# Performance work log

Hardware: AMD Instinct MI355X
Metric: run time of the kernel (lower is better)

Reference implementation:

```python
import jax, jax.numpy as jnp
import numpy as np


def _wkv_scan(key, value, time_decay, time_first):
    # Numerically-stabilized RWKV WKV recurrence; key/value: [B,T,C]
    w = -jnp.exp(time_decay)  # [C]
    B, T, C = key.shape

    def step(carry, kv):
        num, den, mx = carry
        k, v = kv  # [B,C] each
        # output at this timestep
        mo = jnp.maximum(mx, k + time_first)
        e1 = jnp.exp(mx - mo)
        e2 = jnp.exp(k + time_first - mo)
        out = (e1 * num + e2 * v) / (e1 * den + e2)
        # state update
        ms = jnp.maximum(mx + w, k)
        e1s = jnp.exp(mx + w - ms)
        e2s = jnp.exp(k - ms)
        return (e1s * num + e2s * v, e1s * den + e2s, ms), out

    init = (jnp.zeros((B, C), key.dtype),
            jnp.zeros((B, C), key.dtype),
            jnp.full((B, C), -1e38, key.dtype))
    kT = jnp.swapaxes(key, 0, 1)   # [T,B,C]
    vT = jnp.swapaxes(value, 0, 1)
    _, outs = jax.lax.scan(step, init, (kT, vT))
    return jnp.swapaxes(outs, 0, 1)  # [B,T,C]


def setup_inputs() -> dict:
    key = jax.random.key(0)
    ks = jax.random.split(key, 10)
    B, T, C = 8, 2048, 1024
    s = 1.0 / np.sqrt(C)
    return {
        "x": jax.random.normal(ks[0], (B, T, C), jnp.float32),
        "wk": jax.random.normal(ks[1], (C, C), jnp.float32) * s,
        "wv": jax.random.normal(ks[2], (C, C), jnp.float32) * s,
        "wr": jax.random.normal(ks[3], (C, C), jnp.float32) * s,
        "wo": jax.random.normal(ks[4], (C, C), jnp.float32) * s,
        "time_decay": jax.random.normal(ks[5], (C,), jnp.float32) * 0.5,
        "time_first": jax.random.normal(ks[6], (C,), jnp.float32) * 0.5,
        "mix_k": jax.random.uniform(ks[7], (1, 1, C), jnp.float32),
        "mix_v": jax.random.uniform(ks[8], (1, 1, C), jnp.float32),
        "mix_r": jax.random.uniform(ks[9], (1, 1, C), jnp.float32),
    }


def reference(x, wk, wv, wr, wo, time_decay, time_first, mix_k, mix_v, mix_r):
    # time_shift: prev_x[:,0]=0, prev_x[:,t]=x[:,t-1]  (ZeroPad2d((0,0,1,-1)))
    prev_x = jnp.pad(x, ((0, 0), (1, 0), (0, 0)))[:, :-1, :]
    k_in = x * mix_k + prev_x * (1.0 - mix_k)
    v_in = x * mix_v + prev_x * (1.0 - mix_v)
    r_in = x * mix_r + prev_x * (1.0 - mix_r)
    key = jnp.einsum('btc,dc->btd', k_in, wk)
    value = jnp.einsum('btc,dc->btd', v_in, wv)
    receptance = jax.nn.sigmoid(jnp.einsum('btc,dc->btd', r_in, wr))
    wkv = _wkv_scan(key, value, time_decay, time_first)
    rwkv = receptance * wkv
    return jnp.einsum('btc,dc->btd', rwkv, wo)
```

## Files before the change

### kernel.cpp

```cpp
#include <hip/hip_runtime.h>
#include <stdint.h>


using bf16x8 = __attribute__((ext_vector_type(8))) __bf16;
using f32x4  = __attribute__((ext_vector_type(4))) float;

union FU { float f; unsigned int u; };

__device__ __forceinline__ unsigned short f2b(float f) {
  FU v; v.f = f;
  unsigned int u = v.u;
  return (unsigned short)((u + 0x7fffu + ((u >> 16) & 1u)) >> 16);
}
__device__ __forceinline__ float b2f(unsigned short h) {
  FU v; v.u = ((unsigned int)h) << 16; return v.f;
}

__device__ __forceinline__ void gl_lds16(const unsigned short* g,
                                         const unsigned short* l) {
  __builtin_amdgcn_global_load_lds(
      (const __attribute__((address_space(1))) void*)g,
      (__attribute__((address_space(3))) void*)l, 16, 0, 0);
}

#define SBAR()  __builtin_amdgcn_s_barrier()
#define LGKM0() asm volatile("s_waitcnt lgkmcnt(0)")
#define VMW(n)  asm volatile("s_waitcnt vmcnt(" #n ")")

__global__ __launch_bounds__(256) void prep_kernel(
    const float* __restrict__ x,
    const float* __restrict__ w0, const float* __restrict__ w1,
    const float* __restrict__ w2, const float* __restrict__ w3,
    unsigned short* __restrict__ o0, unsigned short* __restrict__ o1,
    unsigned short* __restrict__ o2, unsigned short* __restrict__ o3,
    const float* __restrict__ mk, const float* __restrict__ mv,
    const float* __restrict__ mr,
    unsigned short* __restrict__ ok, unsigned short* __restrict__ ov,
    unsigned short* __restrict__ orr)
{
  int bid = blockIdx.x;
  if (bid < 4096) {
    int mat = bid >> 10, blk = bid & 1023;
    const float* src = (mat == 0) ? w0 : (mat == 1) ? w1 : (mat == 2) ? w2 : w3;
    unsigned short* dst = (mat == 0) ? o0 : (mat == 1) ? o1 : (mat == 2) ? o2 : o3;
    int i = blk * 1024 + threadIdx.x * 4;
    float4 v = *(const float4*)(src + i);
    union { int2 i2; unsigned short u[4]; } o;
    o.u[0] = f2b(v.x); o.u[1] = f2b(v.y); o.u[2] = f2b(v.z); o.u[3] = f2b(v.w);
    *(int2*)(dst + i) = o.i2;
    return;
  }
  int i = (bid - 4096) * 256 + threadIdx.x;
  int base = i * 8;
  int row = base >> 10;
  int t = row & 2047;
  int c = base & 1023;
  float xv[8], pv[8];
  *(float4*)&xv[0] = *(const float4*)(x + base);
  *(float4*)&xv[4] = *(const float4*)(x + base + 4);
  if (t > 0) {
    *(float4*)&pv[0] = *(const float4*)(x + base - 1024);
    *(float4*)&pv[4] = *(const float4*)(x + base - 1024 + 4);
  } else {
#pragma unroll
    for (int e = 0; e < 8; ++e) pv[e] = 0.f;
  }
  float mkv[8], mvv[8], mrv[8];
  *(float4*)&mkv[0] = *(const float4*)(mk + c);
  *(float4*)&mkv[4] = *(const float4*)(mk + c + 4);
  *(float4*)&mvv[0] = *(const float4*)(mv + c);
  *(float4*)&mvv[4] = *(const float4*)(mv + c + 4);
  *(float4*)&mrv[0] = *(const float4*)(mr + c);
  *(float4*)&mrv[4] = *(const float4*)(mr + c + 4);
  union { int4 i4; unsigned short u[8]; } a, b2, d;
#pragma unroll
  for (int e = 0; e < 8; ++e) {
    float xe = xv[e], pe = pv[e];
    a.u[e]  = f2b(xe * mkv[e] + pe * (1.f - mkv[e]));
    b2.u[e] = f2b(xe * mvv[e] + pe * (1.f - mvv[e]));
    d.u[e]  = f2b(xe * mrv[e] + pe * (1.f - mrv[e]));
  }
  *(int4*)(ok + base)  = a.i4;
  *(int4*)(ov + base)  = b2.i4;
  *(int4*)(orr + base) = d.i4;
}


__device__ __forceinline__ void stageHalf(
    const unsigned short* __restrict__ g,
    const unsigned short* l,
    int rh, int kt, int w, int rl, int koffel)
{
#pragma unroll
  for (int c = 0; c < 2; ++c) {
    int rows = rh * 128 + (2 * w + c) * 8;
    gl_lds16(g + (size_t)(rows + rl) * 1024 + kt * 64 + koffel,
             l + rows * 64);
  }
}

template<int Q>
__device__ __forceinline__ void quadMfma(f32x4 (&acc)[8][4],
    bf16x8 a00, bf16x8 a01, bf16x8 a10, bf16x8 a11, bf16x8 (&b)[4][2])
{
#pragma unroll
  for (int j = 0; j < 4; ++j) {
    acc[2*Q][j]   = __builtin_amdgcn_mfma_f32_16x16x32_bf16(a00, b[j][0], acc[2*Q][j],   0, 0, 0);
    acc[2*Q][j]   = __builtin_amdgcn_mfma_f32_16x16x32_bf16(a01, b[j][1], acc[2*Q][j],   0, 0, 0);
    acc[2*Q+1][j] = __builtin_amdgcn_mfma_f32_16x16x32_bf16(a10, b[j][0], acc[2*Q+1][j], 0, 0, 0);
    acc[2*Q+1][j] = __builtin_amdgcn_mfma_f32_16x16x32_bf16(a11, b[j][1], acc[2*Q+1][j], 0, 0, 0);
  }
}

template<bool ST_A, bool ST_B, int VMN>
__device__ __forceinline__ void ktile(
    const unsigned short* aR, const unsigned short* bR,
    const unsigned short* aW, const unsigned short* bW,
    const unsigned short* Am, const unsigned short* Wn,
    int ktA, int ktB, int w, int wm, int wn, int col, int quad,
    int swzel, int rl, int koffel, f32x4 (&acc)[8][4])
{
  const int ks0 = (quad * 8) ^ swzel;
  const int ks1 = (32 + quad * 8) ^ swzel;
  bf16x8 b[4][2];
#pragma unroll
  for (int j = 0; j < 4; ++j) {
    const unsigned short* br = bR + (wn * 64 + j * 16 + col) * 64;
    b[j][0] = *(const bf16x8*)(br + ks0);
    b[j][1] = *(const bf16x8*)(br + ks1);
  }
  const unsigned short* ar = aR + (wm * 128 + col) * 64;
  {
    bf16x8 a00 = *(const bf16x8*)(ar + 0 * 1024 + ks0);
    bf16x8 a01 = *(const bf16x8*)(ar + 0 * 1024 + ks1);
    bf16x8 a10 = *(const bf16x8*)(ar + 1 * 1024 + ks0);
    bf16x8 a11 = *(const bf16x8*)(ar + 1 * 1024 + ks1);
    if (ST_A) stageHalf(Am, aW, 0, ktA, w, rl, koffel);
    SBAR(); LGKM0();
    __builtin_amdgcn_s_setprio(1);
    quadMfma<0>(acc, a00, a01, a10, a11, b);
    __builtin_amdgcn_s_setprio(0);
    SBAR();
  }
  {
    bf16x8 a00 = *(const bf16x8*)(ar + 2 * 1024 + ks0);
    bf16x8 a01 = *(const bf16x8*)(ar + 2 * 1024 + ks1);
    bf16x8 a10 = *(const bf16x8*)(ar + 3 * 1024 + ks0);
    bf16x8 a11 = *(const bf16x8*)(ar + 3 * 1024 + ks1);
    if (ST_A) stageHalf(Am, aW, 1, ktA, w, rl, koffel);
    SBAR(); LGKM0();
    __builtin_amdgcn_s_setprio(1);
    quadMfma<1>(acc, a00, a01, a10, a11, b);
    __builtin_amdgcn_s_setprio(0);
    SBAR();
  }
  {
    bf16x8 a00 = *(const bf16x8*)(ar + 4 * 1024 + ks0);
    bf16x8 a01 = *(const bf16x8*)(ar + 4 * 1024 + ks1);
    bf16x8 a10 = *(const bf16x8*)(ar + 5 * 1024 + ks0);
    bf16x8 a11 = *(const bf16x8*)(ar + 5 * 1024 + ks1);
    if (ST_B) stageHalf(Wn, bW, 0, ktB, w, rl, koffel);
    SBAR(); LGKM0();
    __builtin_amdgcn_s_setprio(1);
    quadMfma<2>(acc, a00, a01, a10, a11, b);
    __builtin_amdgcn_s_setprio(0);
    SBAR();
  }
  {
    bf16x8 a00 = *(const bf16x8*)(ar + 6 * 1024 + ks0);
    bf16x8 a01 = *(const bf16x8*)(ar + 6 * 1024 + ks1);
    bf16x8 a10 = *(const bf16x8*)(ar + 7 * 1024 + ks0);
    bf16x8 a11 = *(const bf16x8*)(ar + 7 * 1024 + ks1);
    if (ST_B) stageHalf(Wn, bW, 1, ktB, w, rl, koffel);
    SBAR(); LGKM0();
    __builtin_amdgcn_s_setprio(1);
    quadMfma<3>(acc, a00, a01, a10, a11, b);
    __builtin_amdgcn_s_setprio(0);
    if constexpr (VMN == 4) { VMW(4); }
    else if constexpr (VMN == 0) { VMW(0); }
    SBAR();
  }
}

template<typename EPI>
__device__ __forceinline__ void gemm256(
    const unsigned short* __restrict__ A,
    const unsigned short* __restrict__ W,
    EPI epi)
{
  __shared__ __align__(16) unsigned short As[2][256 * 64];
  __shared__ __align__(16) unsigned short Bs[2][256 * 64];
  const int tid  = threadIdx.x;
  const int lane = tid & 63;
  const int w    = tid >> 6;
  const int wm   = w >> 2, wn = w & 3;
  const int col  = lane & 15, quad = lane >> 4;
  const int swzel  = (lane & 7) << 3;
  const int rl     = lane >> 3;
  const int koffel = ((lane & 7) ^ rl) << 3;
  const int mBase = blockIdx.x * 256;
  const int nBase = blockIdx.y * 256;
  const unsigned short* Am = A + (size_t)mBase * 1024;
  const unsigned short* Wn = W + (size_t)nBase * 1024;

  f32x4 acc[8][4];
  const f32x4 z = {0.f, 0.f, 0.f, 0.f};
#pragma unroll
  for (int i = 0; i < 8; ++i)
#pragma unroll
    for (int j = 0; j < 4; ++j) acc[i][j] = z;

  stageHalf(Wn, &Bs[0][0], 0, 0, w, rl, koffel);
  stageHalf(Wn, &Bs[0][0], 1, 0, w, rl, koffel);
  stageHalf(Am, &As[0][0], 0, 0, w, rl, koffel);
  stageHalf(Am, &As[0][0], 1, 0, w, rl, koffel);
  stageHalf(Wn, &Bs[1][0], 0, 1, w, rl, koffel);
  stageHalf(Wn, &Bs[1][0], 1, 1, w, rl, koffel);
  VMW(4); SBAR();

#pragma unroll 1
  for (int t = 0; t < 14; t += 2) {
    ktile<true, true, 4>(&As[0][0], &Bs[0][0], &As[1][0], &Bs[0][0],
                         Am, Wn, t + 1, t + 2,
                         w, wm, wn, col, quad, swzel, rl, koffel, acc);
    ktile<true, true, 4>(&As[1][0], &Bs[1][0], &As[0][0], &Bs[1][0],
                         Am, Wn, t + 2, t + 3,
                         w, wm, wn, col, quad, swzel, rl, koffel, acc);
  }
  ktile<true, false, 0>(&As[0][0], &Bs[0][0], &As[1][0], &Bs[0][0],
                        Am, Wn, 15, 0,
                        w, wm, wn, col, quad, swzel, rl, koffel, acc);
  ktile<false, false, -1>(&As[1][0], &Bs[1][0], &As[0][0], &Bs[1][0],
                          Am, Wn, 0, 0,
                          w, wm, wn, col, quad, swzel, rl, koffel, acc);

  const int mB = mBase + wm * 128, nB = nBase + wn * 64;
#pragma unroll
  for (int i = 0; i < 8; ++i)
#pragma unroll
    for (int j = 0; j < 4; ++j)
#pragma unroll
      for (int r = 0; r < 4; ++r)
        epi(mB + i * 16 + quad * 4 + r, nB + j * 16 + col, acc[i][j][r]);
}

__global__ __launch_bounds__(512, 2) void gemmKV2_kernel(
    const unsigned short* __restrict__ A0, const unsigned short* __restrict__ A1,
    const unsigned short* __restrict__ W0, const unsigned short* __restrict__ W1,
    unsigned short* __restrict__ out0, unsigned short* __restrict__ out1)
{
  const int z = blockIdx.z;
  const unsigned short* A = z ? A1 : A0;
  const unsigned short* W = z ? W1 : W0;
  unsigned short* out = z ? out1 : out0;
  gemm256(A, W, [&](int r, int c, float v) {
    out[(size_t)r * 1024 + c] = f2b(v);
  });
}

__global__ __launch_bounds__(512, 2) void gemmR2_kernel(
    const unsigned short* __restrict__ A, const unsigned short* __restrict__ W,
    unsigned short* __restrict__ out)
{
  gemm256(A, W, [&](int r, int c, float v) {
    out[(size_t)r * 1024 + c] = f2b(1.0f / (1.0f + __expf(-v)));
  });
}

__global__ __launch_bounds__(512, 2) void gemmO2_kernel(
    const unsigned short* __restrict__ A, const unsigned short* __restrict__ W,
    float* __restrict__ out)
{
  gemm256(A, W, [&](int r, int c, float v) {
    out[(size_t)r * 1024 + c] = v;
  });
}

__global__ __launch_bounds__(256) void wkv_pass1(
    const unsigned short* __restrict__ kb, const unsigned short* __restrict__ vb,
    const float* __restrict__ td,
    float* __restrict__ snum, float* __restrict__ sden, float* __restrict__ smx,
    int T, int C, int L)
{
  int g = blockIdx.x * 256 + threadIdx.x;
  int bc = g & 8191;
  int ch = g >> 13;
  int c = bc & 1023;
  float w = -__expf(td[c]);
  float num = 0.f, den = 0.f, mx = -1e38f;
  size_t base = ((size_t)(bc >> 10) * T + (size_t)ch * L) * C + c;
  for (int j0 = 0; j0 < L; j0 += 8) {
    float kq[8], vq[8];
#pragma unroll
    for (int j = 0; j < 8; ++j) {
      size_t a = base + (size_t)(j0 + j) * C;
      kq[j] = b2f(kb[a]);
      vq[j] = b2f(vb[a]);
    }
#pragma unroll
    for (int j = 0; j < 8; ++j) {
      float k = kq[j], v = vq[j];
      float mw = mx + w;
      float ms = fmaxf(mw, k);
      float s1 = __expf(mw - ms);
      float s2 = __expf(k - ms);
      num = s1 * num + s2 * v;
      den = s1 * den + s2;
      mx = ms;
    }
  }
  int idx = ch * 8192 + bc;
  snum[idx] = num; sden[idx] = den; smx[idx] = mx;
}

__global__ __launch_bounds__(64) void wkv_pass2(
    const float* __restrict__ snum, const float* __restrict__ sden,
    const float* __restrict__ smx, const float* __restrict__ td,
    float* __restrict__ inum, float* __restrict__ iden, float* __restrict__ imx,
    int L)
{
  int bc = blockIdx.x * 64 + threadIdx.x;
  int c = bc & 1023;
  float Wl = -__expf(td[c]) * (float)L;
  float num = 0.f, den = 0.f, mx = -1e38f;
#pragma unroll
  for (int ch = 0; ch < 32; ++ch) {
    int idx = ch * 8192 + bc;
    inum[idx] = num; iden[idx] = den; imx[idx] = mx;
    float sn = snum[idx], sd = sden[idx], sm = smx[idx];
    float mi = mx + Wl;
    float mo = fmaxf(mi, sm);
    float e1 = __expf(mi - mo);
    float e2 = __expf(sm - mo);
    num = e1 * num + e2 * sn;
    den = e1 * den + e2 * sd;
    mx = mo;
  }
}

__global__ __launch_bounds__(256) void wkv_pass3(
    const unsigned short* __restrict__ kb, const unsigned short* __restrict__ vb,
    const unsigned short* __restrict__ rsig,
    const float* __restrict__ td, const float* __restrict__ tf,
    const float* __restrict__ inum, const float* __restrict__ iden,
    const float* __restrict__ imx,
    unsigned short* __restrict__ rwkv, int T, int C, int L)
{
  int g = blockIdx.x * 256 + threadIdx.x;
  int bc = g & 8191;
  int ch = g >> 13;
  int c = bc & 1023;
  float w = -__expf(td[c]);
  float u = tf[c];
  int idx = ch * 8192 + bc;
  float num = inum[idx], den = iden[idx], mx = imx[idx];
  size_t base = ((size_t)(bc >> 10) * T + (size_t)ch * L) * C + c;
  for (int j0 = 0; j0 < L; j0 += 8) {
    float kq[8], vq[8], rq[8];
#pragma unroll
    for (int j = 0; j < 8; ++j) {
      size_t a = base + (size_t)(j0 + j) * C;
      kq[j] = b2f(kb[a]);
      vq[j] = b2f(vb[a]);
      rq[j] = b2f(rsig[a]);
    }
#pragma unroll
    for (int j = 0; j < 8; ++j) {
      float k = kq[j], v = vq[j];
      float ku = k + u;
      float mo = fmaxf(mx, ku);
      float e1 = __expf(mx - mo);
      float e2 = __expf(ku - mo);
      float o = (e1 * num + e2 * v) / (e1 * den + e2);
      rwkv[base + (size_t)(j0 + j) * C] = f2b(rq[j] * o);
      float mw = mx + w;
      float ms = fmaxf(mw, k);
      float s1 = __expf(mw - ms);
      float s2 = __expf(k - ms);
      num = s1 * num + s2 * v;
      den = s1 * den + s2;
      mx = ms;
    }
  }
}

extern "C" void kernel_launch(void* const* d_in, const int* in_sizes, int n_in,
                              void* d_out, int out_size, void* d_ws, size_t ws_size,
                              hipStream_t stream)
{
  const float* x  = (const float*)d_in[0];
  const float* wk = (const float*)d_in[1];
  const float* wv = (const float*)d_in[2];
  const float* wr = (const float*)d_in[3];
  const float* wo = (const float*)d_in[4];
  const float* td = (const float*)d_in[5];
  const float* tf = (const float*)d_in[6];
  const float* mk = (const float*)d_in[7];
  const float* mv = (const float*)d_in[8];
  const float* mr = (const float*)d_in[9];

  const int B = 8, T = 2048, C = 1024;
  const int M = B * T;
  const int NC = 32, L = 64;
  const size_t MB = 1024 * 1024;

  char* ws = (char*)d_ws;
  unsigned short* bufK = (unsigned short*)(ws);
  unsigned short* bufV = (unsigned short*)(ws + 32 * MB);
  unsigned short* bufR = (unsigned short*)(ws + 64 * MB);
  unsigned short* kb   = (unsigned short*)(ws + 96 * MB);
  unsigned short* wkb  = (unsigned short*)(ws + 128 * MB);
  unsigned short* wvb  = (unsigned short*)(ws + 130 * MB);
  unsigned short* wrb  = (unsigned short*)(ws + 132 * MB);
  unsigned short* wob  = (unsigned short*)(ws + 134 * MB);
  float* snum = (float*)(ws + 136 * MB);
  float* sden = (float*)(ws + 137 * MB);
  float* smx  = (float*)(ws + 138 * MB);
  float* inum = (float*)(ws + 139 * MB);
  float* iden = (float*)(ws + 140 * MB);
  float* imx  = (float*)(ws + 141 * MB);
  unsigned short* vb   = (unsigned short*)(ws + 142 * MB);
  unsigned short* rsig = bufV;
  unsigned short* rwkv = bufR;

  dim3 gKV(M / 256, C / 256, 2);
  dim3 gG(M / 256, C / 256);
  int scanBlocks = (B * C * NC) / 256;

  prep_kernel<<<12288, 256, 0, stream>>>(x, wk, wv, wr, wo, wkb, wvb, wrb, wob,
                                         mk, mv, mr, bufK, bufV, bufR);
  gemmKV2_kernel<<<gKV, 512, 0, stream>>>(bufK, bufV, wkb, wvb, kb, vb);
  gemmR2_kernel<<<gG, 512, 0, stream>>>(bufR, wrb, rsig);
  wkv_pass1<<<scanBlocks, 256, 0, stream>>>(kb, vb, td, snum, sden, smx, T, C, L);
  wkv_pass2<<<(B * C) / 64, 64, 0, stream>>>(snum, sden, smx, td, inum, iden, imx, L);
  wkv_pass3<<<scanBlocks, 256, 0, stream>>>(kb, vb, rsig, td, tf, inum, iden, imx,
                                            rwkv, T, C, L);
  gemmO2_kernel<<<gG, 512, 0, stream>>>(rwkv, wob, (float*)d_out);
}
```

Before: 331.8 us.

## Merge GEMM k-tile phases from four to three and drop redundant barriers

```diff
diff --git a/kernel.cpp b/kernel.cpp
--- a/kernel.cpp
+++ b/kernel.cpp
@@ -24,8 +24,7 @@
 }
 
 #define SBAR()  __builtin_amdgcn_s_barrier()
-#define LGKM0() asm volatile("s_waitcnt lgkmcnt(0)")
-#define VMW(n)  asm volatile("s_waitcnt vmcnt(" #n ")")
+#define VMWC(n) asm volatile("s_waitcnt vmcnt(" #n ")" ::: "memory")
 
 __global__ __launch_bounds__(256) void prep_kernel(
     const float* __restrict__ x,
@@ -112,8 +111,8 @@
   }
 }
 
-template<bool ST_A, bool ST_B, int VMN>
-__device__ __forceinline__ void ktile(
+template<bool ST_A, bool ST_B, int VMN, bool ENDBAR>
+__device__ __forceinline__ void ktile3(
     const unsigned short* aR, const unsigned short* bR,
     const unsigned short* aW, const unsigned short* bW,
     const unsigned short* Am, const unsigned short* Wn,
@@ -122,6 +121,8 @@
 {
   const int ks0 = (quad * 8) ^ swzel;
   const int ks1 = (32 + quad * 8) ^ swzel;
+  const unsigned short* ar = aR + (wm * 128 + col) * 64;
+
   bf16x8 b[4][2];
 #pragma unroll
   for (int j = 0; j < 4; ++j) {
@@ -129,56 +130,50 @@
     b[j][0] = *(const bf16x8*)(br + ks0);
     b[j][1] = *(const bf16x8*)(br + ks1);
   }
-  const unsigned short* ar = aR + (wm * 128 + col) * 64;
   {
     bf16x8 a00 = *(const bf16x8*)(ar + 0 * 1024 + ks0);
     bf16x8 a01 = *(const bf16x8*)(ar + 0 * 1024 + ks1);
     bf16x8 a10 = *(const bf16x8*)(ar + 1 * 1024 + ks0);
     bf16x8 a11 = *(const bf16x8*)(ar + 1 * 1024 + ks1);
-    if (ST_A) stageHalf(Am, aW, 0, ktA, w, rl, koffel);
-    SBAR(); LGKM0();
     __builtin_amdgcn_s_setprio(1);
     quadMfma<0>(acc, a00, a01, a10, a11, b);
     __builtin_amdgcn_s_setprio(0);
     SBAR();
   }
   {
-    bf16x8 a00 = *(const bf16x8*)(ar + 2 * 1024 + ks0);
-    bf16x8 a01 = *(const bf16x8*)(ar + 2 * 1024 + ks1);
-    bf16x8 a10 = *(const bf16x8*)(ar + 3 * 1024 + ks0);
-    bf16x8 a11 = *(const bf16x8*)(ar + 3 * 1024 + ks1);
-    if (ST_A) stageHalf(Am, aW, 1, ktA, w, rl, koffel);
-    SBAR(); LGKM0();
+    bf16x8 a10_ = *(const bf16x8*)(ar + 2 * 1024 + ks0);
+    bf16x8 a11_ = *(const bf16x8*)(ar + 2 * 1024 + ks1);
+    bf16x8 a12_ = *(const bf16x8*)(ar + 3 * 1024 + ks0);
+    bf16x8 a13_ = *(const bf16x8*)(ar + 3 * 1024 + ks1);
+    bf16x8 a20_ = *(const bf16x8*)(ar + 4 * 1024 + ks0);
+    bf16x8 a21_ = *(const bf16x8*)(ar + 4 * 1024 + ks1);
+    bf16x8 a22_ = *(const bf16x8*)(ar + 5 * 1024 + ks0);
+    bf16x8 a23_ = *(const bf16x8*)(ar + 5 * 1024 + ks1);
+    if (ST_A) {
+      stageHalf(Am, aW, 0, ktA, w, rl, koffel);
+      stageHalf(Am, aW, 1, ktA, w, rl, koffel);
+    }
     __builtin_amdgcn_s_setprio(1);
-    quadMfma<1>(acc, a00, a01, a10, a11, b);
+    quadMfma<1>(acc, a10_, a11_, a12_, a13_, b);
+    quadMfma<2>(acc, a20_, a21_, a22_, a23_, b);
     __builtin_amdgcn_s_setprio(0);
     SBAR();
   }
   {
-    bf16x8 a00 = *(const bf16x8*)(ar + 4 * 1024 + ks0);
-    bf16x8 a01 = *(const bf16x8*)(ar + 4 * 1024 + ks1);
-    bf16x8 a10 = *(const bf16x8*)(ar + 5 * 1024 + ks0);
-    bf16x8 a11 = *(const bf16x8*)(ar + 5 * 1024 + ks1);
-    if (ST_B) stageHalf(Wn, bW, 0, ktB, w, rl, koffel);
-    SBAR(); LGKM0();
+    bf16x8 a30_ = *(const bf16x8*)(ar + 6 * 1024 + ks0);
+    bf16x8 a31_ = *(const bf16x8*)(ar + 6 * 1024 + ks1);
+    bf16x8 a32_ = *(const bf16x8*)(ar + 7 * 1024 + ks0);
+    bf16x8 a33_ = *(const bf16x8*)(ar + 7 * 1024 + ks1);
+    if (ST_B) {
+      stageHalf(Wn, bW, 0, ktB, w, rl, koffel);
+      stageHalf(Wn, bW, 1, ktB, w, rl, koffel);
+    }
     __builtin_amdgcn_s_setprio(1);
-    quadMfma<2>(acc, a00, a01, a10, a11, b);
+    quadMfma<3>(acc, a30_, a31_, a32_, a33_, b);
     __builtin_amdgcn_s_setprio(0);
-    SBAR();
-  }
-  {
-    bf16x8 a00 = *(const bf16x8*)(ar + 6 * 1024 + ks0);
-    bf16x8 a01 = *(const bf16x8*)(ar + 6 * 1024 + ks1);
-    bf16x8 a10 = *(const bf16x8*)(ar + 7 * 1024 + ks0);
-    bf16x8 a11 = *(const bf16x8*)(ar + 7 * 1024 + ks1);
-    if (ST_B) stageHalf(Wn, bW, 1, ktB, w, rl, koffel);
-    SBAR(); LGKM0();
-    __builtin_amdgcn_s_setprio(1);
-    quadMfma<3>(acc, a00, a01, a10, a11, b);
-    __builtin_amdgcn_s_setprio(0);
-    if constexpr (VMN == 4) { VMW(4); }
-    else if constexpr (VMN == 0) { VMW(0); }
-    SBAR();
+    if constexpr (VMN == 4) { VMWC(4); }
+    else if constexpr (VMN == 0) { VMWC(0); }
+    if constexpr (ENDBAR) { SBAR(); }
   }
 }
 
@@ -216,23 +211,23 @@
   stageHalf(Am, &As[0][0], 1, 0, w, rl, koffel);
   stageHalf(Wn, &Bs[1][0], 0, 1, w, rl, koffel);
   stageHalf(Wn, &Bs[1][0], 1, 1, w, rl, koffel);
-  VMW(4); SBAR();
+  VMWC(4); SBAR();
 
 #pragma unroll 1
   for (int t = 0; t < 14; t += 2) {
-    ktile<true, true, 4>(&As[0][0], &Bs[0][0], &As[1][0], &Bs[0][0],
-                         Am, Wn, t + 1, t + 2,
-                         w, wm, wn, col, quad, swzel, rl, koffel, acc);
-    ktile<true, true, 4>(&As[1][0], &Bs[1][0], &As[0][0], &Bs[1][0],
-                         Am, Wn, t + 2, t + 3,
-                         w, wm, wn, col, quad, swzel, rl, koffel, acc);
-  }
-  ktile<true, false, 0>(&As[0][0], &Bs[0][0], &As[1][0], &Bs[0][0],
-                        Am, Wn, 15, 0,
-                        w, wm, wn, col, quad, swzel, rl, koffel, acc);
-  ktile<false, false, -1>(&As[1][0], &Bs[1][0], &As[0][0], &Bs[1][0],
-                          Am, Wn, 0, 0,
-                          w, wm, wn, col, quad, swzel, rl, koffel, acc);
+    ktile3<true, true, 4, true>(&As[0][0], &Bs[0][0], &As[1][0], &Bs[0][0],
+                                Am, Wn, t + 1, t + 2,
+                                w, wm, wn, col, quad, swzel, rl, koffel, acc);
+    ktile3<true, true, 4, true>(&As[1][0], &Bs[1][0], &As[0][0], &Bs[1][0],
+                                Am, Wn, t + 2, t + 3,
+                                w, wm, wn, col, quad, swzel, rl, koffel, acc);
+  }
+  ktile3<true, false, 0, true>(&As[0][0], &Bs[0][0], &As[1][0], &Bs[0][0],
+                               Am, Wn, 15, 0,
+                               w, wm, wn, col, quad, swzel, rl, koffel, acc);
+  ktile3<false, false, -1, false>(&As[1][0], &Bs[1][0], &As[0][0], &Bs[1][0],
+                                  Am, Wn, 0, 0,
+                                  w, wm, wn, col, quad, swzel, rl, koffel, acc);
 
   const int mB = mBase + wm * 128, nB = nBase + wn * 64;
 #pragma unroll
```

Result: no change. 333.7 us (+0.6%).

## Fuse time-shift mixing and bf16 conversion into the K/V/R GEMM A-tile staging

Applied to the files above, without the earlier changes.

```diff
diff --git a/kernel.cpp b/kernel.cpp
--- a/kernel.cpp
+++ b/kernel.cpp
@@ -26,63 +26,23 @@
 #define SBAR()  __builtin_amdgcn_s_barrier()
 #define LGKM0() asm volatile("s_waitcnt lgkmcnt(0)")
 #define VMW(n)  asm volatile("s_waitcnt vmcnt(" #n ")")
+#define VMWC(n) asm volatile("s_waitcnt vmcnt(" #n ")" ::: "memory")
 
 __global__ __launch_bounds__(256) void prep_kernel(
-    const float* __restrict__ x,
     const float* __restrict__ w0, const float* __restrict__ w1,
     const float* __restrict__ w2, const float* __restrict__ w3,
     unsigned short* __restrict__ o0, unsigned short* __restrict__ o1,
-    unsigned short* __restrict__ o2, unsigned short* __restrict__ o3,
-    const float* __restrict__ mk, const float* __restrict__ mv,
-    const float* __restrict__ mr,
-    unsigned short* __restrict__ ok, unsigned short* __restrict__ ov,
-    unsigned short* __restrict__ orr)
+    unsigned short* __restrict__ o2, unsigned short* __restrict__ o3)
 {
   int bid = blockIdx.x;
-  if (bid < 4096) {
-    int mat = bid >> 10, blk = bid & 1023;
-    const float* src = (mat == 0) ? w0 : (mat == 1) ? w1 : (mat == 2) ? w2 : w3;
-    unsigned short* dst = (mat == 0) ? o0 : (mat == 1) ? o1 : (mat == 2) ? o2 : o3;
-    int i = blk * 1024 + threadIdx.x * 4;
-    float4 v = *(const float4*)(src + i);
-    union { int2 i2; unsigned short u[4]; } o;
-    o.u[0] = f2b(v.x); o.u[1] = f2b(v.y); o.u[2] = f2b(v.z); o.u[3] = f2b(v.w);
-    *(int2*)(dst + i) = o.i2;
-    return;
-  }
-  int i = (bid - 4096) * 256 + threadIdx.x;
-  int base = i * 8;
-  int row = base >> 10;
-  int t = row & 2047;
-  int c = base & 1023;
-  float xv[8], pv[8];
-  *(float4*)&xv[0] = *(const float4*)(x + base);
-  *(float4*)&xv[4] = *(const float4*)(x + base + 4);
-  if (t > 0) {
-    *(float4*)&pv[0] = *(const float4*)(x + base - 1024);
-    *(float4*)&pv[4] = *(const float4*)(x + base - 1024 + 4);
-  } else {
-#pragma unroll
-    for (int e = 0; e < 8; ++e) pv[e] = 0.f;
-  }
-  float mkv[8], mvv[8], mrv[8];
-  *(float4*)&mkv[0] = *(const float4*)(mk + c);
-  *(float4*)&mkv[4] = *(const float4*)(mk + c + 4);
-  *(float4*)&mvv[0] = *(const float4*)(mv + c);
-  *(float4*)&mvv[4] = *(const float4*)(mv + c + 4);
-  *(float4*)&mrv[0] = *(const float4*)(mr + c);
-  *(float4*)&mrv[4] = *(const float4*)(mr + c + 4);
-  union { int4 i4; unsigned short u[8]; } a, b2, d;
-#pragma unroll
-  for (int e = 0; e < 8; ++e) {
-    float xe = xv[e], pe = pv[e];
-    a.u[e]  = f2b(xe * mkv[e] + pe * (1.f - mkv[e]));
-    b2.u[e] = f2b(xe * mvv[e] + pe * (1.f - mvv[e]));
-    d.u[e]  = f2b(xe * mrv[e] + pe * (1.f - mrv[e]));
-  }
-  *(int4*)(ok + base)  = a.i4;
-  *(int4*)(ov + base)  = b2.i4;
-  *(int4*)(orr + base) = d.i4;
+  int mat = bid >> 10, blk = bid & 1023;
+  const float* src = (mat == 0) ? w0 : (mat == 1) ? w1 : (mat == 2) ? w2 : w3;
+  unsigned short* dst = (mat == 0) ? o0 : (mat == 1) ? o1 : (mat == 2) ? o2 : o3;
+  int i = blk * 1024 + threadIdx.x * 4;
+  float4 v = *(const float4*)(src + i);
+  union { int2 i2; unsigned short u[4]; } o;
+  o.u[0] = f2b(v.x); o.u[1] = f2b(v.y); o.u[2] = f2b(v.z); o.u[3] = f2b(v.w);
+  *(int2*)(dst + i) = o.i2;
 }
 
 
@@ -96,6 +56,45 @@
     int rows = rh * 128 + (2 * w + c) * 8;
     gl_lds16(g + (size_t)(rows + rl) * 1024 + kt * 64 + koffel,
              l + rows * 64);
+  }
+}
+
+__device__ __forceinline__ void stageMixHalf(
+    const float* __restrict__ xg,
+    int mBase, int rh, int kt,
+    float4 ma, float4 mb,
+    unsigned short* lds,
+    int w, int rl, int lq, int koffel)
+{
+#pragma unroll
+  for (int c = 0; c < 2; ++c) {
+    int r = rh * 128 + (2 * w + c) * 8 + rl;
+    const float* xr = xg + (size_t)r * 1024 + kt * 64 + koffel;
+    float4 x0 = *(const float4*)xr;
+    float4 x1 = *(const float4*)(xr + 4);
+    bool t0 = ((mBase + r) & 2047) == 0;
+    const float* pr = t0 ? xr : (xr - 1024);
+    float4 p0 = *(const float4*)pr;
+    float4 p1 = *(const float4*)(pr + 4);
+    if (t0) {
+      p0 = make_float4(0.f, 0.f, 0.f, 0.f);
+      p1 = make_float4(0.f, 0.f, 0.f, 0.f);
+    }
+    float v0 = fmaf(ma.x, x0.x - p0.x, p0.x);
+    float v1 = fmaf(ma.y, x0.y - p0.y, p0.y);
+    float v2 = fmaf(ma.z, x0.z - p0.z, p0.z);
+    float v3 = fmaf(ma.w, x0.w - p0.w, p0.w);
+    float v4 = fmaf(mb.x, x1.x - p1.x, p1.x);
+    float v5 = fmaf(mb.y, x1.y - p1.y, p1.y);
+    float v6 = fmaf(mb.z, x1.z - p1.z, p1.z);
+    float v7 = fmaf(mb.w, x1.w - p1.w, p1.w);
+    unsigned u0, u1, u2, u3;
+    asm("v_cvt_pk_bf16_f32 %0, %1, %2" : "=v"(u0) : "v"(v0), "v"(v1));
+    asm("v_cvt_pk_bf16_f32 %0, %1, %2" : "=v"(u1) : "v"(v2), "v"(v3));
+    asm("v_cvt_pk_bf16_f32 %0, %1, %2" : "=v"(u2) : "v"(v4), "v"(v5));
+    asm("v_cvt_pk_bf16_f32 %0, %1, %2" : "=v"(u3) : "v"(v6), "v"(v7));
+    uint4 o = make_uint4(u0, u1, u2, u3);
+    *(uint4*)(lds + r * 64 + lq * 8) = o;
   }
 }
 
@@ -110,6 +109,149 @@
     acc[2*Q+1][j] = __builtin_amdgcn_mfma_f32_16x16x32_bf16(a10, b[j][0], acc[2*Q+1][j], 0, 0, 0);
     acc[2*Q+1][j] = __builtin_amdgcn_mfma_f32_16x16x32_bf16(a11, b[j][1], acc[2*Q+1][j], 0, 0, 0);
   }
+}
+
+template<bool ST_A, bool ST_B, int VMN>
+__device__ __forceinline__ void ktileMix(
+    const unsigned short* aR, const unsigned short* bR,
+    unsigned short* aW, const unsigned short* bW,
+    const float* __restrict__ xg, const float* __restrict__ mixm, int mBase,
+    const unsigned short* Wn,
+    int ktA, int ktB, int w, int wm, int wn, int col, int quad,
+    int swzel, int rl, int lq, int koffel, f32x4 (&acc)[8][4])
+{
+  const int ks0 = (quad * 8) ^ swzel;
+  const int ks1 = (32 + quad * 8) ^ swzel;
+  float4 ma, mb;
+  if (ST_A) {
+    const float* mp = mixm + ktA * 64 + koffel;
+    ma = *(const float4*)mp;
+    mb = *(const float4*)(mp + 4);
+  }
+  bf16x8 b[4][2];
+#pragma unroll
+  for (int j = 0; j < 4; ++j) {
+    const unsigned short* br = bR + (wn * 64 + j * 16 + col) * 64;
+    b[j][0] = *(const bf16x8*)(br + ks0);
+    b[j][1] = *(const bf16x8*)(br + ks1);
+  }
+  const unsigned short* ar = aR + (wm * 128 + col) * 64;
+  {
+    bf16x8 a00 = *(const bf16x8*)(ar + 0 * 1024 + ks0);
+    bf16x8 a01 = *(const bf16x8*)(ar + 0 * 1024 + ks1);
+    bf16x8 a10 = *(const bf16x8*)(ar + 1 * 1024 + ks0);
+    bf16x8 a11 = *(const bf16x8*)(ar + 1 * 1024 + ks1);
+    if (ST_A) stageMixHalf(xg, mBase, 0, ktA, ma, mb, aW, w, rl, lq, koffel);
+    SBAR(); LGKM0();
+    __builtin_amdgcn_s_setprio(1);
+    quadMfma<0>(acc, a00, a01, a10, a11, b);
+    __builtin_amdgcn_s_setprio(0);
+    SBAR();
+  }
+  {
+    bf16x8 a00 = *(const bf16x8*)(ar + 2 * 1024 + ks0);
+    bf16x8 a01 = *(const bf16x8*)(ar + 2 * 1024 + ks1);
+    bf16x8 a10 = *(const bf16x8*)(ar + 3 * 1024 + ks0);
+    bf16x8 a11 = *(const bf16x8*)(ar + 3 * 1024 + ks1);
+    if (ST_A) stageMixHalf(xg, mBase, 1, ktA, ma, mb, aW, w, rl, lq, koffel);
+    SBAR(); LGKM0();
+    __builtin_amdgcn_s_setprio(1);
+    quadMfma<1>(acc, a00, a01, a10, a11, b);
+    __builtin_amdgcn_s_setprio(0);
+    SBAR();
+  }
+  {
+    bf16x8 a00 = *(const bf16x8*)(ar + 4 * 1024 + ks0);
+    bf16x8 a01 = *(const bf16x8*)(ar + 4 * 1024 + ks1);
+    bf16x8 a10 = *(const bf16x8*)(ar + 5 * 1024 + ks0);
+    bf16x8 a11 = *(const bf16x8*)(ar + 5 * 1024 + ks1);
+    if (ST_B) stageHalf(Wn, bW, 0, ktB, w, rl, koffel);
+    SBAR(); LGKM0();
+    __builtin_amdgcn_s_setprio(1);
+    quadMfma<2>(acc, a00, a01, a10, a11, b);
+    __builtin_amdgcn_s_setprio(0);
+    SBAR();
+  }
+  {
+    bf16x8 a00 = *(const bf16x8*)(ar + 6 * 1024 + ks0);
+    bf16x8 a01 = *(const bf16x8*)(ar + 6 * 1024 + ks1);
+    bf16x8 a10 = *(const bf16x8*)(ar + 7 * 1024 + ks0);
+    bf16x8 a11 = *(const bf16x8*)(ar + 7 * 1024 + ks1);
+    if (ST_B) stageHalf(Wn, bW, 1, ktB, w, rl, koffel);
+    SBAR(); LGKM0();
+    __builtin_amdgcn_s_setprio(1);
+    quadMfma<3>(acc, a00, a01, a10, a11, b);
+    __builtin_amdgcn_s_setprio(0);
+    if constexpr (VMN == 4) { VMWC(4); }
+    else if constexpr (VMN == 0) { VMWC(0); }
+    SBAR();
+  }
+}
+
+template<typename EPI>
+__device__ __forceinline__ void gemm256mix(
+    const float* __restrict__ x, const float* __restrict__ mixm,
+    const unsigned short* __restrict__ W, EPI epi)
+{
+  __shared__ __align__(16) unsigned short As[2][256 * 64];
+  __shared__ __align__(16) unsigned short Bs[2][256 * 64];
+  const int tid  = threadIdx.x;
+  const int lane = tid & 63;
+  const int w    = tid >> 6;
+  const int wm   = w >> 2, wn = w & 3;
+  const int col  = lane & 15, quad = lane >> 4;
+  const int lq     = lane & 7;
+  const int rl     = lane >> 3;
+  const int swzel  = lq << 3;
+  const int koffel = (lq ^ rl) << 3;
+  const int mBase = blockIdx.x * 256;
+  const int nBase = blockIdx.y * 256;
+  const float* xg = x + (size_t)mBase * 1024;
+  const unsigned short* Wn = W + (size_t)nBase * 1024;
+
+  f32x4 acc[8][4];
+  const f32x4 z = {0.f, 0.f, 0.f, 0.f};
+#pragma unroll
+  for (int i = 0; i < 8; ++i)
+#pragma unroll
+    for (int j = 0; j < 4; ++j) acc[i][j] = z;
+
+  stageHalf(Wn, &Bs[0][0], 0, 0, w, rl, koffel);
+  stageHalf(Wn, &Bs[0][0], 1, 0, w, rl, koffel);
+  stageHalf(Wn, &Bs[1][0], 0, 1, w, rl, koffel);
+  stageHalf(Wn, &Bs[1][0], 1, 1, w, rl, koffel);
+  {
+    const float* mp = mixm + koffel;
+    float4 ma = *(const float4*)mp, mb = *(const float4*)(mp + 4);
+    stageMixHalf(xg, mBase, 0, 0, ma, mb, &As[0][0], w, rl, lq, koffel);
+    stageMixHalf(xg, mBase, 1, 0, ma, mb, &As[0][0], w, rl, lq, koffel);
+  }
+  VMWC(4); LGKM0(); SBAR();
+
+#pragma unroll 1
+  for (int t = 0; t < 14; t += 2) {
+    ktileMix<true, true, 4>(&As[0][0], &Bs[0][0], &As[1][0], &Bs[0][0],
+                            xg, mixm, mBase, Wn, t + 1, t + 2,
+                            w, wm, wn, col, quad, swzel, rl, lq, koffel, acc);
+    ktileMix<true, true, 4>(&As[1][0], &Bs[1][0], &As[0][0], &Bs[1][0],
+                            xg, mixm, mBase, Wn, t + 2, t + 3,
+                            w, wm, wn, col, quad, swzel, rl, lq, koffel, acc);
+  }
+  ktileMix<true, false, 0>(&As[0][0], &Bs[0][0], &As[1][0], &Bs[0][0],
+                           xg, mixm, mBase, Wn, 15, 0,
+                           w, wm, wn, col, quad, swzel, rl, lq, koffel, acc);
+  ktileMix<false, false, -1>(&As[1][0], &Bs[1][0], &As[0][0], &Bs[1][0],
+                             xg, mixm, mBase, Wn, 0, 0,
+                             w, wm, wn, col, quad, swzel, rl, lq, koffel, acc);
+
+  const int mB = mBase + wm * 128, nB = nBase + wn * 64;
+#pragma unroll
+  for (int i = 0; i < 8; ++i)
+#pragma unroll
+    for (int j = 0; j < 4; ++j)
+#pragma unroll
+      for (int r = 0; r < 4; ++r)
+        epi(mB + i * 16 + quad * 4 + r, nB + j * 16 + col, acc[i][j][r]);
 }
 
 template<bool ST_A, bool ST_B, int VMN>
@@ -244,25 +386,26 @@
         epi(mB + i * 16 + quad * 4 + r, nB + j * 16 + col, acc[i][j][r]);
 }
 
-__global__ __launch_bounds__(512, 2) void gemmKV2_kernel(
-    const unsigned short* __restrict__ A0, const unsigned short* __restrict__ A1,
+__global__ __launch_bounds__(512, 2) void gemmKVmix_kernel(
+    const float* __restrict__ x,
+    const float* __restrict__ mk, const float* __restrict__ mv,
     const unsigned short* __restrict__ W0, const unsigned short* __restrict__ W1,
     unsigned short* __restrict__ out0, unsigned short* __restrict__ out1)
 {
   const int z = blockIdx.z;
-  const unsigned short* A = z ? A1 : A0;
+  const float* mixm = z ? mv : mk;
   const unsigned short* W = z ? W1 : W0;
   unsigned short* out = z ? out1 : out0;
-  gemm256(A, W, [&](int r, int c, float v) {
+  gemm256mix(x, mixm, W, [&](int r, int c, float v) {
     out[(size_t)r * 1024 + c] = f2b(v);
   });
 }
 
-__global__ __launch_bounds__(512, 2) void gemmR2_kernel(
-    const unsigned short* __restrict__ A, const unsigned short* __restrict__ W,
-    unsigned short* __restrict__ out)
-{
-  gemm256(A, W, [&](int r, int c, float v) {
+__global__ __launch_bounds__(512, 2) void gemmRmix_kernel(
+    const float* __restrict__ x, const float* __restrict__ mr,
+    const unsigned short* __restrict__ W, unsigned short* __restrict__ out)
+{
+  gemm256mix(x, mr, W, [&](int r, int c, float v) {
     out[(size_t)r * 1024 + c] = f2b(1.0f / (1.0f + __expf(-v)));
   });
 }
@@ -371,7 +514,7 @@
       float mo = fmaxf(mx, ku);
       float e1 = __expf(mx - mo);
       float e2 = __expf(ku - mo);
-      float o = (e1 * num + e2 * v) / (e1 * den + e2);
+      float o = __fdividef(e1 * num + e2 * v, e1 * den + e2);
       rwkv[base + (size_t)(j0 + j) * C] = f2b(rq[j] * o);
       float mw = mx + w;
       float ms = fmaxf(mw, k);
@@ -405,9 +548,8 @@
   const size_t MB = 1024 * 1024;
 
   char* ws = (char*)d_ws;
-  unsigned short* bufK = (unsigned short*)(ws);
-  unsigned short* bufV = (unsigned short*)(ws + 32 * MB);
-  unsigned short* bufR = (unsigned short*)(ws + 64 * MB);
+  unsigned short* rsig = (unsigned short*)(ws + 32 * MB);
+  unsigned short* rwkv = (unsigned short*)(ws + 64 * MB);
   unsigned short* kb   = (unsigned short*)(ws + 96 * MB);
   unsigned short* wkb  = (unsigned short*)(ws + 128 * MB);
   unsigned short* wvb  = (unsigned short*)(ws + 130 * MB);
@@ -420,17 +562,14 @@
   float* iden = (float*)(ws + 140 * MB);
   float* imx  = (float*)(ws + 141 * MB);
   unsigned short* vb   = (unsigned short*)(ws + 142 * MB);
-  unsigned short* rsig = bufV;
-  unsigned short* rwkv = bufR;
 
   dim3 gKV(M / 256, C / 256, 2);
   dim3 gG(M / 256, C / 256);
   int scanBlocks = (B * C * NC) / 256;
 
-  prep_kernel<<<12288, 256, 0, stream>>>(x, wk, wv, wr, wo, wkb, wvb, wrb, wob,
-                                         mk, mv, mr, bufK, bufV, bufR);
-  gemmKV2_kernel<<<gKV, 512, 0, stream>>>(bufK, bufV, wkb, wvb, kb, vb);
-  gemmR2_kernel<<<gG, 512, 0, stream>>>(bufR, wrb, rsig);
+  prep_kernel<<<4096, 256, 0, stream>>>(wk, wv, wr, wo, wkb, wvb, wrb, wob);
+  gemmKVmix_kernel<<<gKV, 512, 0, stream>>>(x, mk, mv, wkb, wvb, kb, vb);
+  gemmRmix_kernel<<<gG, 512, 0, stream>>>(x, mr, wrb, rsig);
   wkv_pass1<<<scanBlocks, 256, 0, stream>>>(kb, vb, td, snum, sden, smx, T, C, L);
   wkv_pass2<<<(B * C) / 64, 64, 0, stream>>>(snum, sden, smx, td, inum, iden, imx, L);
   wkv_pass3<<<scanBlocks, 256, 0, stream>>>(kb, vb, rsig, td, tf, inum, iden, imx,
```

After: 415.1 us. 1.25x slower.

## Double chunk count in WKV scan and software-pipeline bf16 loads

Applied to the files above, without the earlier changes.

```diff
diff --git a/kernel.cpp b/kernel.cpp
--- a/kernel.cpp
+++ b/kernel.cpp
@@ -276,11 +276,12 @@
   });
 }
 
+
 __global__ __launch_bounds__(256) void wkv_pass1(
     const unsigned short* __restrict__ kb, const unsigned short* __restrict__ vb,
     const float* __restrict__ td,
     float* __restrict__ snum, float* __restrict__ sden, float* __restrict__ smx,
-    int T, int C, int L)
+    int T, int C)
 {
   int g = blockIdx.x * 256 + threadIdx.x;
   int bc = g & 8191;
@@ -288,23 +289,44 @@
   int c = bc & 1023;
   float w = -__expf(td[c]);
   float num = 0.f, den = 0.f, mx = -1e38f;
-  size_t base = ((size_t)(bc >> 10) * T + (size_t)ch * L) * C + c;
-  for (int j0 = 0; j0 < L; j0 += 8) {
-    float kq[8], vq[8];
-#pragma unroll
-    for (int j = 0; j < 8; ++j) {
-      size_t a = base + (size_t)(j0 + j) * C;
-      kq[j] = b2f(kb[a]);
-      vq[j] = b2f(vb[a]);
-    }
-#pragma unroll
-    for (int j = 0; j < 8; ++j) {
-      float k = kq[j], v = vq[j];
+  size_t base = ((size_t)(bc >> 10) * 2048 + (size_t)ch * 32) * 1024 + c;
+  float ka[8], va[8], kc[8], vc[8];
+#pragma unroll
+  for (int j = 0; j < 8; ++j) {
+    size_t a = base + (size_t)j * 1024;
+    ka[j] = b2f(kb[a]); va[j] = b2f(vb[a]);
+  }
+#pragma unroll
+  for (int j0 = 0; j0 < 32; j0 += 16) {
+#pragma unroll
+    for (int j = 0; j < 8; ++j) {
+      size_t a = base + (size_t)(j0 + 8 + j) * 1024;
+      kc[j] = b2f(kb[a]); vc[j] = b2f(vb[a]);
+    }
+#pragma unroll
+    for (int j = 0; j < 8; ++j) {
       float mw = mx + w;
-      float ms = fmaxf(mw, k);
+      float ms = fmaxf(mw, ka[j]);
       float s1 = __expf(mw - ms);
-      float s2 = __expf(k - ms);
-      num = s1 * num + s2 * v;
+      float s2 = __expf(ka[j] - ms);
+      num = s1 * num + s2 * va[j];
+      den = s1 * den + s2;
+      mx = ms;
+    }
+    if (j0 + 16 < 32) {
+#pragma unroll
+      for (int j = 0; j < 8; ++j) {
+        size_t a = base + (size_t)(j0 + 16 + j) * 1024;
+        ka[j] = b2f(kb[a]); va[j] = b2f(vb[a]);
+      }
+    }
+#pragma unroll
+    for (int j = 0; j < 8; ++j) {
+      float mw = mx + w;
+      float ms = fmaxf(mw, kc[j]);
+      float s1 = __expf(mw - ms);
+      float s2 = __expf(kc[j] - ms);
+      num = s1 * num + s2 * vc[j];
       den = s1 * den + s2;
       mx = ms;
     }
@@ -316,15 +338,14 @@
 __global__ __launch_bounds__(64) void wkv_pass2(
     const float* __restrict__ snum, const float* __restrict__ sden,
     const float* __restrict__ smx, const float* __restrict__ td,
-    float* __restrict__ inum, float* __restrict__ iden, float* __restrict__ imx,
-    int L)
+    float* __restrict__ inum, float* __restrict__ iden, float* __restrict__ imx)
 {
   int bc = blockIdx.x * 64 + threadIdx.x;
   int c = bc & 1023;
-  float Wl = -__expf(td[c]) * (float)L;
+  float Wl = -__expf(td[c]) * 32.0f;
   float num = 0.f, den = 0.f, mx = -1e38f;
 #pragma unroll
-  for (int ch = 0; ch < 32; ++ch) {
+  for (int ch = 0; ch < 64; ++ch) {
     int idx = ch * 8192 + bc;
     inum[idx] = num; iden[idx] = den; imx[idx] = mx;
     float sn = snum[idx], sd = sden[idx], sm = smx[idx];
@@ -344,7 +365,7 @@
     const float* __restrict__ td, const float* __restrict__ tf,
     const float* __restrict__ inum, const float* __restrict__ iden,
     const float* __restrict__ imx,
-    unsigned short* __restrict__ rwkv, int T, int C, int L)
+    unsigned short* __restrict__ rwkv, int T, int C)
 {
   int g = blockIdx.x * 256 + threadIdx.x;
   int bc = g & 8191;
@@ -354,25 +375,53 @@
   float u = tf[c];
   int idx = ch * 8192 + bc;
   float num = inum[idx], den = iden[idx], mx = imx[idx];
-  size_t base = ((size_t)(bc >> 10) * T + (size_t)ch * L) * C + c;
-  for (int j0 = 0; j0 < L; j0 += 8) {
-    float kq[8], vq[8], rq[8];
-#pragma unroll
-    for (int j = 0; j < 8; ++j) {
-      size_t a = base + (size_t)(j0 + j) * C;
-      kq[j] = b2f(kb[a]);
-      vq[j] = b2f(vb[a]);
-      rq[j] = b2f(rsig[a]);
-    }
-#pragma unroll
-    for (int j = 0; j < 8; ++j) {
-      float k = kq[j], v = vq[j];
+  size_t base = ((size_t)(bc >> 10) * 2048 + (size_t)ch * 32) * 1024 + c;
+  float ka[8], va[8], ra[8], kc[8], vc[8], rc[8];
+#pragma unroll
+  for (int j = 0; j < 8; ++j) {
+    size_t a = base + (size_t)j * 1024;
+    ka[j] = b2f(kb[a]); va[j] = b2f(vb[a]); ra[j] = b2f(rsig[a]);
+  }
+#pragma unroll
+  for (int j0 = 0; j0 < 32; j0 += 16) {
+#pragma unroll
+    for (int j = 0; j < 8; ++j) {
+      size_t a = base + (size_t)(j0 + 8 + j) * 1024;
+      kc[j] = b2f(kb[a]); vc[j] = b2f(vb[a]); rc[j] = b2f(rsig[a]);
+    }
+#pragma unroll
+    for (int j = 0; j < 8; ++j) {
+      float k = ka[j], v = va[j];
       float ku = k + u;
       float mo = fmaxf(mx, ku);
       float e1 = __expf(mx - mo);
       float e2 = __expf(ku - mo);
-      float o = (e1 * num + e2 * v) / (e1 * den + e2);
-      rwkv[base + (size_t)(j0 + j) * C] = f2b(rq[j] * o);
+      float o = __fdividef(e1 * num + e2 * v, e1 * den + e2);
+      rwkv[base + (size_t)(j0 + j) * 1024] = f2b(ra[j] * o);
+      float mw = mx + w;
+      float ms = fmaxf(mw, k);
+      float s1 = __expf(mw - ms);
+      float s2 = __expf(k - ms);
+      num = s1 * num + s2 * v;
+      den = s1 * den + s2;
+      mx = ms;
+    }
+    if (j0 + 16 < 32) {
+#pragma unroll
+      for (int j = 0; j < 8; ++j) {
+        size_t a = base + (size_t)(j0 + 16 + j) * 1024;
+        ka[j] = b2f(kb[a]); va[j] = b2f(vb[a]); ra[j] = b2f(rsig[a]);
+      }
+    }
+#pragma unroll
+    for (int j = 0; j < 8; ++j) {
+      float k = kc[j], v = vc[j];
+      float ku = k + u;
+      float mo = fmaxf(mx, ku);
+      float e1 = __expf(mx - mo);
+      float e2 = __expf(ku - mo);
+      float o = __fdividef(e1 * num + e2 * v, e1 * den + e2);
+      rwkv[base + (size_t)(j0 + 8 + j) * 1024] = f2b(rc[j] * o);
       float mw = mx + w;
       float ms = fmaxf(mw, k);
       float s1 = __expf(mw - ms);
@@ -401,7 +450,7 @@
 
   const int B = 8, T = 2048, C = 1024;
   const int M = B * T;
-  const int NC = 32, L = 64;
+  const int NC = 64;
   const size_t MB = 1024 * 1024;
 
   char* ws = (char*)d_ws;
@@ -413,13 +462,13 @@
   unsigned short* wvb  = (unsigned short*)(ws + 130 * MB);
   unsigned short* wrb  = (unsigned short*)(ws + 132 * MB);
   unsigned short* wob  = (unsigned short*)(ws + 134 * MB);
-  float* snum = (float*)(ws + 136 * MB);
-  float* sden = (float*)(ws + 137 * MB);
-  float* smx  = (float*)(ws + 138 * MB);
-  float* inum = (float*)(ws + 139 * MB);
-  float* iden = (float*)(ws + 140 * MB);
-  float* imx  = (float*)(ws + 141 * MB);
   unsigned short* vb   = (unsigned short*)(ws + 142 * MB);
+  float* snum = (float*)(ws + 0 * MB);
+  float* sden = (float*)(ws + 2 * MB);
+  float* smx  = (float*)(ws + 4 * MB);
+  float* inum = (float*)(ws + 6 * MB);
+  float* iden = (float*)(ws + 8 * MB);
+  float* imx  = (float*)(ws + 10 * MB);
   unsigned short* rsig = bufV;
   unsigned short* rwkv = bufR;
 
@@ -431,9 +480,9 @@
                                          mk, mv, mr, bufK, bufV, bufR);
   gemmKV2_kernel<<<gKV, 512, 0, stream>>>(bufK, bufV, wkb, wvb, kb, vb);
   gemmR2_kernel<<<gG, 512, 0, stream>>>(bufR, wrb, rsig);
-  wkv_pass1<<<scanBlocks, 256, 0, stream>>>(kb, vb, td, snum, sden, smx, T, C, L);
-  wkv_pass2<<<(B * C) / 64, 64, 0, stream>>>(snum, sden, smx, td, inum, iden, imx, L);
+  wkv_pass1<<<scanBlocks, 256, 0, stream>>>(kb, vb, td, snum, sden, smx, T, C);
+  wkv_pass2<<<(B * C) / 64, 64, 0, stream>>>(snum, sden, smx, td, inum, iden, imx);
   wkv_pass3<<<scanBlocks, 256, 0, stream>>>(kb, vb, rsig, td, tf, inum, iden, imx,
-                                            rwkv, T, C, L);
+                                            rwkv, T, C);
   gemmO2_kernel<<<gG, 512, 0, stream>>>(rwkv, wob, (float*)d_out);
 }
```

Result: slower. 356.9 us (+7.6%).
